# Optimization experiments

Hardware: AMD Instinct MI355X
Metric: run time of the kernel (lower is better)

## Reference

```python
import jax, jax.numpy as jnp
import numpy as np

N_NODES = 50000
N_EDGES = 600000
IN_DIM = 128
HID_DIM = 128


def setup_inputs() -> dict:
    key = jax.random.key(0)
    k_h, k_src, k_dst, k_w1, k_b1, k_w2, k_b2 = jax.random.split(key, 7)
    h = jax.random.normal(k_h, (N_NODES, IN_DIM), dtype=jnp.float32)
    src = jax.random.randint(k_src, (N_EDGES,), 0, N_NODES, dtype=jnp.int32)
    dst = jax.random.randint(k_dst, (N_EDGES,), 0, N_NODES, dtype=jnp.int32)
    # Edge MLP params: Linear(in_dim, out_dim) -> ReLU -> Linear(out_dim, 1) -> ReLU
    s1 = 1.0 / np.sqrt(IN_DIM)
    s2 = 1.0 / np.sqrt(HID_DIM)
    W1 = jax.random.uniform(k_w1, (IN_DIM, HID_DIM), jnp.float32, -s1, s1)
    b1 = jax.random.uniform(k_b1, (HID_DIM,), jnp.float32, -s1, s1)
    W2 = jax.random.uniform(k_w2, (HID_DIM, 1), jnp.float32, -s2, s2)
    b2 = jax.random.uniform(k_b2, (1,), jnp.float32, -s2, s2)
    return {"h": h, "src": src, "dst": dst, "W1": W1, "b1": b1, "W2": W2, "b2": b2}


def reference(h, src, dst, W1, b1, W2, b2):
    n_nodes = h.shape[0]
    # Edge MLP on feature differences (gather src/dst node features)
    dif = h[src] - h[dst]                                   # [E, D]
    hidden = jax.nn.relu(dif @ W1 + b1)                      # [E, H]
    att = jax.nn.relu(hidden @ W2 + b2)[:, 0]                # [E]
    att = jax.nn.sigmoid(att)                                # [E]
    # EdgeWeightNorm('right') on reversed graph: divide by the sum of
    # attention weights over edges sharing the same ORIGINAL source node.
    denom = jax.ops.segment_sum(att, src, num_segments=n_nodes)  # [N]
    w = att / denom[src]                                     # [E]
    # Message: w_e * src features, sum-aggregated at destination nodes
    msg = w[:, None] * h[src]                                # [E, D]
    out = jax.ops.segment_sum(msg, dst, num_segments=n_nodes)  # [N, D]
    return out
```

## Files before the change

kernel.cpp:

```cpp
#include <hip/hip_runtime.h>


typedef unsigned int uint;
typedef unsigned short ushort;
typedef __attribute__((ext_vector_type(8))) short short8;
typedef __attribute__((ext_vector_type(4))) float f32x4;
typedef __attribute__((ext_vector_type(2))) _Float16 h2;

static __device__ __forceinline__ uint pack_f16(float a, float b) {
  _Float16 ha = (_Float16)a, hb = (_Float16)b;
  unsigned short ua = __builtin_bit_cast(unsigned short, ha);
  unsigned short ub = __builtin_bit_cast(unsigned short, hb);
  return ((uint)ub << 16) | ua;
}
static __device__ __forceinline__ float2 unpack_f16(uint u) {
  _Float16 lo = __builtin_bit_cast(_Float16, (unsigned short)(u & 0xffffu));
  _Float16 hi = __builtin_bit_cast(_Float16, (unsigned short)(u >> 16));
  return make_float2((float)lo, (float)hi);
}
static __device__ __forceinline__ h2 as_h2(uint u) { return __builtin_bit_cast(h2, u); }
static __device__ __forceinline__ h2 relu2(h2 a) {
  h2 r;
  r.x = a.x > (_Float16)0 ? a.x : (_Float16)0;
  r.y = a.y > (_Float16)0 ? a.y : (_Float16)0;
  return r;
}
static __device__ __forceinline__ float dot2acc(h2 a, h2 b, float c) {
#if __has_builtin(__builtin_amdgcn_fdot2)
  return __builtin_amdgcn_fdot2(a, b, c, false);
#else
  return c + (float)a.x * (float)b.x + (float)a.y * (float)b.y;
#endif
}
static __device__ __forceinline__ ushort f2bf(float x) {
  uint u = __float_as_uint(x);
  u += 0x7fffu + ((u >> 16) & 1u);
  return (ushort)(u >> 16);
}

__global__ __launch_bounds__(256) void k_prep(const float* __restrict__ W1,
                                              ushort* __restrict__ w1t_swz,
                                              int* __restrict__ zbase, int zwords) {
  int b = blockIdx.x;
  if (b < 64) {
    int idx = b * 256 + threadIdx.x;
    int n = idx >> 7, k = idx & 127;
    float v = W1[k * 128 + n];
    int byte_off = n * 256 + ((k * 2) ^ ((n & 7) << 4));
    w1t_swz[byte_off >> 1] = f2bf(v);
  } else {
    int i = (b - 64) * 256 + threadIdx.x;
    int stride = (gridDim.x - 64) * 256;
    for (; i < zwords; i += stride) zbase[i] = 0;
  }
}

__global__ __launch_bounds__(256) void k_gemm(const float* __restrict__ h,
                                              const ushort* __restrict__ w1t_swz,
                                              uint* __restrict__ gh,
                                              uint4* __restrict__ hh4,
                                              int n_nodes,
                                              const int* __restrict__ dst,
                                              int* __restrict__ counts,
                                              int n_edges, int gemm_blocks) {
  if ((int)blockIdx.x >= gemm_blocks) {
    int hb = blockIdx.x - gemm_blocks;
    int i = hb * 256 + threadIdx.x;
    int stride = (gridDim.x - gemm_blocks) * 256;
    for (int e = i; e < n_edges; e += stride) atomicAdd(&counts[dst[e]], 1);
    return;
  }
  __shared__ ushort w1s[16384];
  int tid = threadIdx.x;
  {
    const uint4* srcw = (const uint4*)w1t_swz;
    uint4* dstw = (uint4*)w1s;
    #pragma unroll
    for (int i = 0; i < 8; ++i) dstw[tid + 256 * i] = srcw[tid + 256 * i];
  }
  __syncthreads();
  int wave = tid >> 6, lane = tid & 63;
  int tile = blockIdx.x * 4 + wave;
  if (tile * 16 >= n_nodes) return;
  int n0 = tile * 16;
  int l15 = lane & 15, kq = lane >> 4;
  int row = n0 + l15;

  f32x4 acc[8];
  #pragma unroll
  for (int ct = 0; ct < 8; ++ct) acc[ct] = (f32x4){0.f, 0.f, 0.f, 0.f};

  #pragma unroll
  for (int kb = 0; kb < 4; ++kb) {
    const float* hp = &h[(size_t)row * 128 + kb * 32 + kq * 8];
    float4 p0 = *(const float4*)hp;
    float4 p1 = *(const float4*)(hp + 4);
    short8 a;
    a[0] = (short)f2bf(p0.x); a[1] = (short)f2bf(p0.y);
    a[2] = (short)f2bf(p0.z); a[3] = (short)f2bf(p0.w);
    a[4] = (short)f2bf(p1.x); a[5] = (short)f2bf(p1.y);
    a[6] = (short)f2bf(p1.z); a[7] = (short)f2bf(p1.w);
    uint4 hv;
    hv.x = pack_f16(p0.x, p0.y); hv.y = pack_f16(p0.z, p0.w);
    hv.z = pack_f16(p1.x, p1.y); hv.w = pack_f16(p1.z, p1.w);
    hh4[(size_t)row * 16 + kb * 4 + kq] = hv;
    #pragma unroll
    for (int ct = 0; ct < 8; ++ct) {
      int n = ct * 16 + l15;
      int byte_off = n * 256 + (((kb * 64) + kq * 16) ^ ((n & 7) << 4));
      short8 b = *(const short8*)((const char*)w1s + byte_off);
      acc[ct] = __builtin_amdgcn_mfma_f32_16x16x32_bf16(a, b, acc[ct], 0, 0, 0);
    }
  }
  ushort* gh16 = (ushort*)gh;
  #pragma unroll
  for (int ct = 0; ct < 8; ++ct) {
    #pragma unroll
    for (int r = 0; r < 4; ++r) {
      int orow = n0 + kq * 4 + r;
      _Float16 v = (_Float16)acc[ct][r];
      gh16[(size_t)orow * 128 + ct * 16 + l15] = __builtin_bit_cast(unsigned short, v);
    }
  }
}

__global__ __launch_bounds__(256) void k_scanA(const int* __restrict__ counts,
                                               int* __restrict__ partials,
                                               int n, int chunk) {
  __shared__ int red[256];
  int b = blockIdx.x, t = threadIdx.x;
  int idx = b * chunk + t;
  red[t] = (t < chunk && idx < n) ? counts[idx] : 0;
  __syncthreads();
  for (int off = 128; off > 0; off >>= 1) {
    if (t < off) red[t] += red[t + off];
    __syncthreads();
  }
  if (t == 0) partials[b] = red[0];
}

__global__ __launch_bounds__(256) void k_scanB(int* __restrict__ partials,
                                               int* __restrict__ row_start,
                                               int n, int total) {
  __shared__ int p[256];
  int t = threadIdx.x;
  int orig = partials[t];
  p[t] = orig;
  __syncthreads();
  #pragma unroll
  for (int off = 1; off < 256; off <<= 1) {
    int v = (t >= off) ? p[t - off] : 0;
    __syncthreads();
    p[t] += v;
    __syncthreads();
  }
  partials[t] = p[t] - orig;
  if (t == 0) row_start[n] = total;
}

__global__ __launch_bounds__(256) void k_scanC(int* __restrict__ counts,
                                               const int* __restrict__ partials,
                                               int* __restrict__ row_start,
                                               int n, int chunk) {
  __shared__ int p[256];
  int b = blockIdx.x, t = threadIdx.x;
  int idx = b * chunk + t;
  bool ok = (t < chunk && idx < n);
  int orig = ok ? counts[idx] : 0;
  p[t] = orig;
  __syncthreads();
  #pragma unroll
  for (int off = 1; off < 256; off <<= 1) {
    int v = (t >= off) ? p[t - off] : 0;
    __syncthreads();
    p[t] += v;
    __syncthreads();
  }
  if (ok) {
    row_start[idx] = partials[b] + p[t] - orig;
    counts[idx] = 0;
  }
}

__global__ __launch_bounds__(256) void k_fill0(const int* __restrict__ src,
                                               const int* __restrict__ dst,
                                               const int* __restrict__ row_start,
                                               int* __restrict__ cursor,
                                               int* __restrict__ bsrc,
                                               int n_edges) {
  int i = blockIdx.x * blockDim.x + threadIdx.x;
  int stride = gridDim.x * blockDim.x;
  for (int e = i; e < n_edges; e += stride) {
    int d = dst[e];
    int pos = atomicAdd(&cursor[d], 1);
    bsrc[row_start[d] + pos] = src[e];
  }
}

__global__ __launch_bounds__(256) void k_att2(const uint4* __restrict__ gh4,
                                              const int* __restrict__ bsrc,
                                              const int* __restrict__ row_start,
                                              const float* __restrict__ b1,
                                              const float* __restrict__ W2,
                                              const float* __restrict__ b2,
                                              int2* __restrict__ bucket,
                                              float* __restrict__ denom,
                                              int n_nodes) {
  int lane = threadIdx.x & 63;
  int sub = lane >> 4, l16 = lane & 15;
  int d = blockIdx.x * 4 + (threadIdx.x >> 6);
  if (d >= n_nodes) return;
  int beg = row_start[d], end = row_start[d + 1];
  if (beg == end) return;
  float4 b1a = *(const float4*)&b1[l16 * 8];
  float4 b1b = *(const float4*)&b1[l16 * 8 + 4];
  float4 w2a = *(const float4*)&W2[l16 * 8];
  float4 w2b = *(const float4*)&W2[l16 * 8 + 4];
  float b2v = b2[0];
  uint4 ud = gh4[(size_t)d * 16 + l16];
  float2 d0 = unpack_f16(ud.x), d1 = unpack_f16(ud.y);
  float2 d2 = unpack_f16(ud.z), d3 = unpack_f16(ud.w);
  h2 c0, c1, c2, c3, wh0, wh1, wh2, wh3;
  c0.x = (_Float16)(b1a.x - d0.x); c0.y = (_Float16)(b1a.y - d0.y);
  c1.x = (_Float16)(b1a.z - d1.x); c1.y = (_Float16)(b1a.w - d1.y);
  c2.x = (_Float16)(b1b.x - d2.x); c2.y = (_Float16)(b1b.y - d2.y);
  c3.x = (_Float16)(b1b.z - d3.x); c3.y = (_Float16)(b1b.w - d3.y);
  wh0.x = (_Float16)w2a.x; wh0.y = (_Float16)w2a.y;
  wh1.x = (_Float16)w2a.z; wh1.y = (_Float16)w2a.w;
  wh2.x = (_Float16)w2b.x; wh2.y = (_Float16)w2b.y;
  wh3.x = (_Float16)w2b.z; wh3.y = (_Float16)w2b.w;
  for (int jb = beg; jb < end; jb += 8) {
    int j0 = jb + sub, j1 = jb + sub + 4;
    bool v0 = j0 < end, v1 = j1 < end;
    int s0 = 0, s1 = 0;
    float acc0 = 0.f, acc1 = 0.f;
    if (v0) s0 = bsrc[j0];
    if (v1) s1 = bsrc[j1];
    uint4 ua, ub;
    if (v0) ua = gh4[(size_t)s0 * 16 + l16];
    if (v1) ub = gh4[(size_t)s1 * 16 + l16];
    if (v0) {
      acc0 = dot2acc(relu2(as_h2(ua.x) + c0), wh0, acc0);
      acc0 = dot2acc(relu2(as_h2(ua.y) + c1), wh1, acc0);
      acc0 = dot2acc(relu2(as_h2(ua.z) + c2), wh2, acc0);
      acc0 = dot2acc(relu2(as_h2(ua.w) + c3), wh3, acc0);
    }
    if (v1) {
      acc1 = dot2acc(relu2(as_h2(ub.x) + c0), wh0, acc1);
      acc1 = dot2acc(relu2(as_h2(ub.y) + c1), wh1, acc1);
      acc1 = dot2acc(relu2(as_h2(ub.z) + c2), wh2, acc1);
      acc1 = dot2acc(relu2(as_h2(ub.w) + c3), wh3, acc1);
    }
    acc0 += __shfl_xor(acc0, 1); acc1 += __shfl_xor(acc1, 1);
    acc0 += __shfl_xor(acc0, 2); acc1 += __shfl_xor(acc1, 2);
    acc0 += __shfl_xor(acc0, 4); acc1 += __shfl_xor(acc1, 4);
    acc0 += __shfl_xor(acc0, 8); acc1 += __shfl_xor(acc1, 8);
    if (l16 == 0) {
      if (v0) {
        float a = fmaxf(acc0 + b2v, 0.f);
        a = 1.f / (1.f + __expf(-a));
        bucket[j0] = make_int2(s0, __float_as_int(a));
        atomicAdd(&denom[s0], a);
      }
      if (v1) {
        float a = fmaxf(acc1 + b2v, 0.f);
        a = 1.f / (1.f + __expf(-a));
        bucket[j1] = make_int2(s1, __float_as_int(a));
        atomicAdd(&denom[s1], a);
      }
    }
  }
}

__global__ __launch_bounds__(256) void k_agg(const uint4* __restrict__ hh4,
                                             const int* __restrict__ row_start,
                                             const int2* __restrict__ bucket,
                                             const float* __restrict__ denom,
                                             float* __restrict__ out, int n_nodes) {
  int lane = threadIdx.x & 63;
  int sub = lane >> 4, l16 = lane & 15;
  int d = blockIdx.x * 4 + (threadIdx.x >> 6);
  if (d >= n_nodes) return;
  int beg = row_start[d], end = row_start[d + 1];
  int cnt = end - beg;
  float a0 = 0.f, a1 = 0.f, a2 = 0.f, a3 = 0.f;
  float a4 = 0.f, a5 = 0.f, a6 = 0.f, a7 = 0.f;
  for (int base = 0; base < cnt; base += 64) {
    int nb = cnt - base; if (nb > 64) nb = 64;
    int2 ew = make_int2(0, 0);
    if (lane < nb) {
      ew = bucket[beg + base + lane];
      float w = __int_as_float(ew.y) / denom[ew.x];
      ew.y = __float_as_int(w);
    }
    int steps = (nb + 3) >> 2;
    int jj = 0;
    for (; jj + 2 <= steps; jj += 2) {
      int i0 = jj * 4 + sub, i1 = i0 + 4;
      int sA = __shfl(ew.x, i0), sB = __shfl(ew.x, i1);
      float wA = __int_as_float(__shfl(ew.y, i0));
      float wB = __int_as_float(__shfl(ew.y, i1));
      bool vA = i0 < nb, vB = i1 < nb;
      uint4 va, vb;
      if (vA) va = hh4[(size_t)sA * 16 + l16];
      if (vB) vb = hh4[(size_t)sB * 16 + l16];
      if (vA) {
        float2 f0 = unpack_f16(va.x), f1 = unpack_f16(va.y);
        float2 f2 = unpack_f16(va.z), f3 = unpack_f16(va.w);
        a0 = fmaf(wA, f0.x, a0); a1 = fmaf(wA, f0.y, a1);
        a2 = fmaf(wA, f1.x, a2); a3 = fmaf(wA, f1.y, a3);
        a4 = fmaf(wA, f2.x, a4); a5 = fmaf(wA, f2.y, a5);
        a6 = fmaf(wA, f3.x, a6); a7 = fmaf(wA, f3.y, a7);
      }
      if (vB) {
        float2 f0 = unpack_f16(vb.x), f1 = unpack_f16(vb.y);
        float2 f2 = unpack_f16(vb.z), f3 = unpack_f16(vb.w);
        a0 = fmaf(wB, f0.x, a0); a1 = fmaf(wB, f0.y, a1);
        a2 = fmaf(wB, f1.x, a2); a3 = fmaf(wB, f1.y, a3);
        a4 = fmaf(wB, f2.x, a4); a5 = fmaf(wB, f2.y, a5);
        a6 = fmaf(wB, f3.x, a6); a7 = fmaf(wB, f3.y, a7);
      }
    }
    if (jj < steps) {
      int i0 = jj * 4 + sub;
      int sA = __shfl(ew.x, i0);
      float wA = __int_as_float(__shfl(ew.y, i0));
      if (i0 < nb) {
        uint4 va = hh4[(size_t)sA * 16 + l16];
        float2 f0 = unpack_f16(va.x), f1 = unpack_f16(va.y);
        float2 f2 = unpack_f16(va.z), f3 = unpack_f16(va.w);
        a0 = fmaf(wA, f0.x, a0); a1 = fmaf(wA, f0.y, a1);
        a2 = fmaf(wA, f1.x, a2); a3 = fmaf(wA, f1.y, a3);
        a4 = fmaf(wA, f2.x, a4); a5 = fmaf(wA, f2.y, a5);
        a6 = fmaf(wA, f3.x, a6); a7 = fmaf(wA, f3.y, a7);
      }
    }
  }
  #pragma unroll
  for (int off = 16; off < 64; off <<= 1) {
    a0 += __shfl_xor(a0, off); a1 += __shfl_xor(a1, off);
    a2 += __shfl_xor(a2, off); a3 += __shfl_xor(a3, off);
    a4 += __shfl_xor(a4, off); a5 += __shfl_xor(a5, off);
    a6 += __shfl_xor(a6, off); a7 += __shfl_xor(a7, off);
  }
  if (sub == 0) {
    *(float4*)&out[(size_t)d * 128 + l16 * 8]     = make_float4(a0, a1, a2, a3);
    *(float4*)&out[(size_t)d * 128 + l16 * 8 + 4] = make_float4(a4, a5, a6, a7);
  }
}

extern "C" void kernel_launch(void* const* d_in, const int* in_sizes, int n_in,
                              void* d_out, int out_size, void* d_ws, size_t ws_size,
                              hipStream_t stream) {
  const float* h   = (const float*)d_in[0];
  const int*   src = (const int*)d_in[1];
  const int*   dst = (const int*)d_in[2];
  const float* W1  = (const float*)d_in[3];
  const float* b1  = (const float*)d_in[4];
  const float* W2  = (const float*)d_in[5];
  const float* b2  = (const float*)d_in[6];
  float* out = (float*)d_out;

  int n_nodes = in_sizes[0] / 128;
  int n_edges = in_sizes[1];

  char* ws = (char*)d_ws;
  uint*   gh        = (uint*)ws;
  uint*   hh        = gh + (size_t)n_nodes * 64;
  float*  denom     = (float*)(hh + (size_t)n_nodes * 64);
  int*    counts    = (int*)(denom + n_nodes);
  int*    row_start = counts + n_nodes;
  int*    partials  = row_start + n_nodes + 1;
  ushort* w1t       = (ushort*)(partials + 256);
  int*    bsrc      = (int*)(w1t + 16384);
  int2*   bucket    = (int2*)(((uintptr_t)(bsrc + n_edges) + 15) & ~(uintptr_t)15);

  int chunk = (n_nodes + 255) / 256;
  int n_tiles = (n_nodes + 15) / 16;
  int gemm_blocks = (n_tiles + 3) / 4;
  int nblk4 = (n_nodes + 3) / 4;
  k_prep <<<64 + 16, 256, 0, stream>>>(W1, w1t, (int*)denom, 2 * n_nodes);
  k_gemm <<<gemm_blocks + 256, 256, 0, stream>>>(h, w1t, gh, (uint4*)hh, n_nodes,
                                                 dst, counts, n_edges, gemm_blocks);
  k_scanA<<<256, 256, 0, stream>>>(counts, partials, n_nodes, chunk);
  k_scanB<<<1, 256, 0, stream>>>(partials, row_start, n_nodes, n_edges);
  k_scanC<<<256, 256, 0, stream>>>(counts, partials, row_start, n_nodes, chunk);
  k_fill0<<<1024, 256, 0, stream>>>(src, dst, row_start, counts, bsrc, n_edges);
  k_att2 <<<nblk4, 256, 0, stream>>>((const uint4*)gh, bsrc, row_start, b1, W2, b2,
                                     bucket, denom, n_nodes);
  k_agg  <<<nblk4, 256, 0, stream>>>((const uint4*)hh, row_start, bucket, denom, out, n_nodes);
}
```

Before: 155.6 us.

## Assign one node per quarter-wave, record atomic ranks, merge scan kernels

The counting pass now saves each edge's atomic rank, so the CSR fill no longer needs a second atomic pass or a cursor reset. The two later scan kernels are merged, with every block redoing the 256-entry partial scan, which removes one launch. The attention and aggregation kernels map each destination node to 16 lanes instead of a full wave, so 16 nodes share a block and the cross-subgroup shuffle reductions go away. This is meant to cut wasted lanes at an average degree of about 12, at the cost of serial per-node loops and divergence between nodes of different degree within a wave.

```diff
diff --git a/kernel.cpp b/kernel.cpp
--- a/kernel.cpp
+++ b/kernel.cpp
@@ -62,12 +62,16 @@
                                               int n_nodes,
                                               const int* __restrict__ dst,
                                               int* __restrict__ counts,
+                                              int* __restrict__ rank,
                                               int n_edges, int gemm_blocks) {
   if ((int)blockIdx.x >= gemm_blocks) {
     int hb = blockIdx.x - gemm_blocks;
     int i = hb * 256 + threadIdx.x;
     int stride = (gridDim.x - gemm_blocks) * 256;
-    for (int e = i; e < n_edges; e += stride) atomicAdd(&counts[dst[e]], 1);
+    for (int e = i; e < n_edges; e += stride) {
+      int r = atomicAdd(&counts[dst[e]], 1);
+      rank[e] = r;
+    }
     return;
   }
   __shared__ ushort w1s[16384];
@@ -139,31 +143,23 @@
   if (t == 0) partials[b] = red[0];
 }
 
-__global__ __launch_bounds__(256) void k_scanB(int* __restrict__ partials,
-                                               int* __restrict__ row_start,
-                                               int n, int total) {
-  __shared__ int p[256];
-  int t = threadIdx.x;
-  int orig = partials[t];
-  p[t] = orig;
-  __syncthreads();
-  #pragma unroll
-  for (int off = 1; off < 256; off <<= 1) {
-    int v = (t >= off) ? p[t - off] : 0;
-    __syncthreads();
-    p[t] += v;
-    __syncthreads();
-  }
-  partials[t] = p[t] - orig;
-  if (t == 0) row_start[n] = total;
-}
-
-__global__ __launch_bounds__(256) void k_scanC(int* __restrict__ counts,
-                                               const int* __restrict__ partials,
-                                               int* __restrict__ row_start,
-                                               int n, int chunk) {
+__global__ __launch_bounds__(256) void k_scanC2(const int* __restrict__ counts,
+                                                const int* __restrict__ partials,
+                                                int* __restrict__ row_start,
+                                                int n, int chunk, int total) {
+  __shared__ int bp[256];
   __shared__ int p[256];
   int b = blockIdx.x, t = threadIdx.x;
+  bp[t] = partials[t];
+  __syncthreads();
+  #pragma unroll
+  for (int off = 1; off < 256; off <<= 1) {
+    int v = (t >= off) ? bp[t - off] : 0;
+    __syncthreads();
+    bp[t] += v;
+    __syncthreads();
+  }
+  int base = (b == 0) ? 0 : bp[b - 1];
   int idx = b * chunk + t;
   bool ok = (t < chunk && idx < n);
   int orig = ok ? counts[idx] : 0;
@@ -176,24 +172,20 @@
     p[t] += v;
     __syncthreads();
   }
-  if (ok) {
-    row_start[idx] = partials[b] + p[t] - orig;
-    counts[idx] = 0;
-  }
+  if (ok) row_start[idx] = base + p[t] - orig;
+  if (b == 0 && t == 0) row_start[n] = total;
 }
 
 __global__ __launch_bounds__(256) void k_fill0(const int* __restrict__ src,
                                                const int* __restrict__ dst,
                                                const int* __restrict__ row_start,
-                                               int* __restrict__ cursor,
+                                               const int* __restrict__ rank,
                                                int* __restrict__ bsrc,
                                                int n_edges) {
   int i = blockIdx.x * blockDim.x + threadIdx.x;
   int stride = gridDim.x * blockDim.x;
   for (int e = i; e < n_edges; e += stride) {
-    int d = dst[e];
-    int pos = atomicAdd(&cursor[d], 1);
-    bsrc[row_start[d] + pos] = src[e];
+    bsrc[row_start[dst[e]] + rank[e]] = src[e];
   }
 }
 
@@ -208,43 +200,43 @@
                                               int n_nodes) {
   int lane = threadIdx.x & 63;
   int sub = lane >> 4, l16 = lane & 15;
-  int d = blockIdx.x * 4 + (threadIdx.x >> 6);
-  if (d >= n_nodes) return;
-  int beg = row_start[d], end = row_start[d + 1];
-  if (beg == end) return;
+  int wavei = threadIdx.x >> 6;
+  int d = blockIdx.x * 16 + wavei * 4 + sub;
+  int beg = 0, end = 0;
+  if (d < n_nodes) { beg = row_start[d]; end = row_start[d + 1]; }
   float4 b1a = *(const float4*)&b1[l16 * 8];
   float4 b1b = *(const float4*)&b1[l16 * 8 + 4];
   float4 w2a = *(const float4*)&W2[l16 * 8];
   float4 w2b = *(const float4*)&W2[l16 * 8 + 4];
   float b2v = b2[0];
-  uint4 ud = gh4[(size_t)d * 16 + l16];
-  float2 d0 = unpack_f16(ud.x), d1 = unpack_f16(ud.y);
-  float2 d2 = unpack_f16(ud.z), d3 = unpack_f16(ud.w);
   h2 c0, c1, c2, c3, wh0, wh1, wh2, wh3;
-  c0.x = (_Float16)(b1a.x - d0.x); c0.y = (_Float16)(b1a.y - d0.y);
-  c1.x = (_Float16)(b1a.z - d1.x); c1.y = (_Float16)(b1a.w - d1.y);
-  c2.x = (_Float16)(b1b.x - d2.x); c2.y = (_Float16)(b1b.y - d2.y);
-  c3.x = (_Float16)(b1b.z - d3.x); c3.y = (_Float16)(b1b.w - d3.y);
   wh0.x = (_Float16)w2a.x; wh0.y = (_Float16)w2a.y;
   wh1.x = (_Float16)w2a.z; wh1.y = (_Float16)w2a.w;
   wh2.x = (_Float16)w2b.x; wh2.y = (_Float16)w2b.y;
   wh3.x = (_Float16)w2b.z; wh3.y = (_Float16)w2b.w;
-  for (int jb = beg; jb < end; jb += 8) {
-    int j0 = jb + sub, j1 = jb + sub + 4;
-    bool v0 = j0 < end, v1 = j1 < end;
-    int s0 = 0, s1 = 0;
+  c0 = (h2)(_Float16)0; c1 = c0; c2 = c0; c3 = c0;
+  if (beg < end) {
+    uint4 ud = gh4[(size_t)d * 16 + l16];
+    float2 d0 = unpack_f16(ud.x), d1 = unpack_f16(ud.y);
+    float2 d2 = unpack_f16(ud.z), d3 = unpack_f16(ud.w);
+    c0.x = (_Float16)(b1a.x - d0.x); c0.y = (_Float16)(b1a.y - d0.y);
+    c1.x = (_Float16)(b1a.z - d1.x); c1.y = (_Float16)(b1a.w - d1.y);
+    c2.x = (_Float16)(b1b.x - d2.x); c2.y = (_Float16)(b1b.y - d2.y);
+    c3.x = (_Float16)(b1b.z - d3.x); c3.y = (_Float16)(b1b.w - d3.y);
+  }
+  for (int j0 = beg; j0 < end; j0 += 2) {
+    int j1 = j0 + 1;
+    bool v1 = j1 < end;
+    int s0 = bsrc[j0];
+    int s1 = v1 ? bsrc[j1] : 0;
+    uint4 ua = gh4[(size_t)s0 * 16 + l16];
+    uint4 ub;
+    if (v1) ub = gh4[(size_t)s1 * 16 + l16];
     float acc0 = 0.f, acc1 = 0.f;
-    if (v0) s0 = bsrc[j0];
-    if (v1) s1 = bsrc[j1];
-    uint4 ua, ub;
-    if (v0) ua = gh4[(size_t)s0 * 16 + l16];
-    if (v1) ub = gh4[(size_t)s1 * 16 + l16];
-    if (v0) {
-      acc0 = dot2acc(relu2(as_h2(ua.x) + c0), wh0, acc0);
-      acc0 = dot2acc(relu2(as_h2(ua.y) + c1), wh1, acc0);
-      acc0 = dot2acc(relu2(as_h2(ua.z) + c2), wh2, acc0);
-      acc0 = dot2acc(relu2(as_h2(ua.w) + c3), wh3, acc0);
-    }
+    acc0 = dot2acc(relu2(as_h2(ua.x) + c0), wh0, acc0);
+    acc0 = dot2acc(relu2(as_h2(ua.y) + c1), wh1, acc0);
+    acc0 = dot2acc(relu2(as_h2(ua.z) + c2), wh2, acc0);
+    acc0 = dot2acc(relu2(as_h2(ua.w) + c3), wh3, acc0);
     if (v1) {
       acc1 = dot2acc(relu2(as_h2(ub.x) + c0), wh0, acc1);
       acc1 = dot2acc(relu2(as_h2(ub.y) + c1), wh1, acc1);
@@ -256,17 +248,15 @@
     acc0 += __shfl_xor(acc0, 4); acc1 += __shfl_xor(acc1, 4);
     acc0 += __shfl_xor(acc0, 8); acc1 += __shfl_xor(acc1, 8);
     if (l16 == 0) {
-      if (v0) {
-        float a = fmaxf(acc0 + b2v, 0.f);
-        a = 1.f / (1.f + __expf(-a));
-        bucket[j0] = make_int2(s0, __float_as_int(a));
-        atomicAdd(&denom[s0], a);
-      }
+      float a = fmaxf(acc0 + b2v, 0.f);
+      a = 1.f / (1.f + __expf(-a));
+      bucket[j0] = make_int2(s0, __float_as_int(a));
+      atomicAdd(&denom[s0], a);
       if (v1) {
-        float a = fmaxf(acc1 + b2v, 0.f);
-        a = 1.f / (1.f + __expf(-a));
-        bucket[j1] = make_int2(s1, __float_as_int(a));
-        atomicAdd(&denom[s1], a);
+        float a1 = fmaxf(acc1 + b2v, 0.f);
+        a1 = 1.f / (1.f + __expf(-a1));
+        bucket[j1] = make_int2(s1, __float_as_int(a1));
+        atomicAdd(&denom[s1], a1);
       }
     }
   }
@@ -279,71 +269,40 @@
                                              float* __restrict__ out, int n_nodes) {
   int lane = threadIdx.x & 63;
   int sub = lane >> 4, l16 = lane & 15;
-  int d = blockIdx.x * 4 + (threadIdx.x >> 6);
-  if (d >= n_nodes) return;
-  int beg = row_start[d], end = row_start[d + 1];
-  int cnt = end - beg;
+  int wavei = threadIdx.x >> 6;
+  int d = blockIdx.x * 16 + wavei * 4 + sub;
+  int beg = 0, end = 0;
+  if (d < n_nodes) { beg = row_start[d]; end = row_start[d + 1]; }
   float a0 = 0.f, a1 = 0.f, a2 = 0.f, a3 = 0.f;
   float a4 = 0.f, a5 = 0.f, a6 = 0.f, a7 = 0.f;
-  for (int base = 0; base < cnt; base += 64) {
-    int nb = cnt - base; if (nb > 64) nb = 64;
-    int2 ew = make_int2(0, 0);
-    if (lane < nb) {
-      ew = bucket[beg + base + lane];
-      float w = __int_as_float(ew.y) / denom[ew.x];
-      ew.y = __float_as_int(w);
-    }
-    int steps = (nb + 3) >> 2;
-    int jj = 0;
-    for (; jj + 2 <= steps; jj += 2) {
-      int i0 = jj * 4 + sub, i1 = i0 + 4;
-      int sA = __shfl(ew.x, i0), sB = __shfl(ew.x, i1);
-      float wA = __int_as_float(__shfl(ew.y, i0));
-      float wB = __int_as_float(__shfl(ew.y, i1));
-      bool vA = i0 < nb, vB = i1 < nb;
-      uint4 va, vb;
-      if (vA) va = hh4[(size_t)sA * 16 + l16];
-      if (vB) vb = hh4[(size_t)sB * 16 + l16];
-      if (vA) {
-        float2 f0 = unpack_f16(va.x), f1 = unpack_f16(va.y);
-        float2 f2 = unpack_f16(va.z), f3 = unpack_f16(va.w);
-        a0 = fmaf(wA, f0.x, a0); a1 = fmaf(wA, f0.y, a1);
-        a2 = fmaf(wA, f1.x, a2); a3 = fmaf(wA, f1.y, a3);
-        a4 = fmaf(wA, f2.x, a4); a5 = fmaf(wA, f2.y, a5);
-        a6 = fmaf(wA, f3.x, a6); a7 = fmaf(wA, f3.y, a7);
-      }
-      if (vB) {
-        float2 f0 = unpack_f16(vb.x), f1 = unpack_f16(vb.y);
-        float2 f2 = unpack_f16(vb.z), f3 = unpack_f16(vb.w);
-        a0 = fmaf(wB, f0.x, a0); a1 = fmaf(wB, f0.y, a1);
-        a2 = fmaf(wB, f1.x, a2); a3 = fmaf(wB, f1.y, a3);
-        a4 = fmaf(wB, f2.x, a4); a5 = fmaf(wB, f2.y, a5);
-        a6 = fmaf(wB, f3.x, a6); a7 = fmaf(wB, f3.y, a7);
-      }
-    }
-    if (jj < steps) {
-      int i0 = jj * 4 + sub;
-      int sA = __shfl(ew.x, i0);
-      float wA = __int_as_float(__shfl(ew.y, i0));
-      if (i0 < nb) {
-        uint4 va = hh4[(size_t)sA * 16 + l16];
-        float2 f0 = unpack_f16(va.x), f1 = unpack_f16(va.y);
-        float2 f2 = unpack_f16(va.z), f3 = unpack_f16(va.w);
-        a0 = fmaf(wA, f0.x, a0); a1 = fmaf(wA, f0.y, a1);
-        a2 = fmaf(wA, f1.x, a2); a3 = fmaf(wA, f1.y, a3);
-        a4 = fmaf(wA, f2.x, a4); a5 = fmaf(wA, f2.y, a5);
-        a6 = fmaf(wA, f3.x, a6); a7 = fmaf(wA, f3.y, a7);
-      }
-    }
-  }
-  #pragma unroll
-  for (int off = 16; off < 64; off <<= 1) {
-    a0 += __shfl_xor(a0, off); a1 += __shfl_xor(a1, off);
-    a2 += __shfl_xor(a2, off); a3 += __shfl_xor(a3, off);
-    a4 += __shfl_xor(a4, off); a5 += __shfl_xor(a5, off);
-    a6 += __shfl_xor(a6, off); a7 += __shfl_xor(a7, off);
-  }
-  if (sub == 0) {
+  for (int j0 = beg; j0 < end; j0 += 2) {
+    int j1 = j0 + 1;
+    bool v1 = j1 < end;
+    int2 e0 = bucket[j0];
+    int2 e1 = v1 ? bucket[j1] : make_int2(0, 0);
+    float w0 = __int_as_float(e0.y) / denom[e0.x];
+    float w1 = v1 ? __int_as_float(e1.y) / denom[e1.x] : 0.f;
+    uint4 va = hh4[(size_t)e0.x * 16 + l16];
+    uint4 vb;
+    if (v1) vb = hh4[(size_t)e1.x * 16 + l16];
+    {
+      float2 f0 = unpack_f16(va.x), f1 = unpack_f16(va.y);
+      float2 f2 = unpack_f16(va.z), f3 = unpack_f16(va.w);
+      a0 = fmaf(w0, f0.x, a0); a1 = fmaf(w0, f0.y, a1);
+      a2 = fmaf(w0, f1.x, a2); a3 = fmaf(w0, f1.y, a3);
+      a4 = fmaf(w0, f2.x, a4); a5 = fmaf(w0, f2.y, a5);
+      a6 = fmaf(w0, f3.x, a6); a7 = fmaf(w0, f3.y, a7);
+    }
+    if (v1) {
+      float2 f0 = unpack_f16(vb.x), f1 = unpack_f16(vb.y);
+      float2 f2 = unpack_f16(vb.z), f3 = unpack_f16(vb.w);
+      a0 = fmaf(w1, f0.x, a0); a1 = fmaf(w1, f0.y, a1);
+      a2 = fmaf(w1, f1.x, a2); a3 = fmaf(w1, f1.y, a3);
+      a4 = fmaf(w1, f2.x, a4); a5 = fmaf(w1, f2.y, a5);
+      a6 = fmaf(w1, f3.x, a6); a7 = fmaf(w1, f3.y, a7);
+    }
+  }
+  if (d < n_nodes) {
     *(float4*)&out[(size_t)d * 128 + l16 * 8]     = make_float4(a0, a1, a2, a3);
     *(float4*)&out[(size_t)d * 128 + l16 * 8 + 4] = make_float4(a4, a5, a6, a7);
   }
@@ -373,20 +332,20 @@
   int*    partials  = row_start + n_nodes + 1;
   ushort* w1t       = (ushort*)(partials + 256);
   int*    bsrc      = (int*)(w1t + 16384);
-  int2*   bucket    = (int2*)(((uintptr_t)(bsrc + n_edges) + 15) & ~(uintptr_t)15);
+  int*    rank      = bsrc + n_edges;
+  int2*   bucket    = (int2*)(((uintptr_t)(rank + n_edges) + 15) & ~(uintptr_t)15);
 
   int chunk = (n_nodes + 255) / 256;
   int n_tiles = (n_nodes + 15) / 16;
   int gemm_blocks = (n_tiles + 3) / 4;
-  int nblk4 = (n_nodes + 3) / 4;
-  k_prep <<<64 + 16, 256, 0, stream>>>(W1, w1t, (int*)denom, 2 * n_nodes);
-  k_gemm <<<gemm_blocks + 256, 256, 0, stream>>>(h, w1t, gh, (uint4*)hh, n_nodes,
-                                                 dst, counts, n_edges, gemm_blocks);
-  k_scanA<<<256, 256, 0, stream>>>(counts, partials, n_nodes, chunk);
-  k_scanB<<<1, 256, 0, stream>>>(partials, row_start, n_nodes, n_edges);
-  k_scanC<<<256, 256, 0, stream>>>(counts, partials, row_start, n_nodes, chunk);
-  k_fill0<<<1024, 256, 0, stream>>>(src, dst, row_start, counts, bsrc, n_edges);
-  k_att2 <<<nblk4, 256, 0, stream>>>((const uint4*)gh, bsrc, row_start, b1, W2, b2,
-                                     bucket, denom, n_nodes);
-  k_agg  <<<nblk4, 256, 0, stream>>>((const uint4*)hh, row_start, bucket, denom, out, n_nodes);
-}
+  int nblk16 = (n_nodes + 15) / 16;
+  k_prep  <<<64 + 16, 256, 0, stream>>>(W1, w1t, (int*)denom, 2 * n_nodes);
+  k_gemm  <<<gemm_blocks + 256, 256, 0, stream>>>(h, w1t, gh, (uint4*)hh, n_nodes,
+                                                  dst, counts, rank, n_edges, gemm_blocks);
+  k_scanA <<<256, 256, 0, stream>>>(counts, partials, n_nodes, chunk);
+  k_scanC2<<<256, 256, 0, stream>>>(counts, partials, row_start, n_nodes, chunk, n_edges);
+  k_fill0 <<<1024, 256, 0, stream>>>(src, dst, row_start, rank, bsrc, n_edges);
+  k_att2  <<<nblk16, 256, 0, stream>>>((const uint4*)gh, bsrc, row_start, b1, W2, b2,
+                                       bucket, denom, n_nodes);
+  k_agg   <<<nblk16, 256, 0, stream>>>((const uint4*)hh, row_start, bucket, denom, out, n_nodes);
+}
```

Measured after the change: 135.8 us. 1.15x faster.
